# Kernel optimization log

Measured on AMD Instinct MI355X. Metric: run time of the kernel, lower is better.

## Reference

```python
import jax, jax.numpy as jnp
import numpy as np

DIM = 512
NUM_HEADS = 8
HEAD_DIM = DIM // NUM_HEADS
LN_EPS = 1e-5


def setup_inputs() -> dict:
    key = jax.random.key(0)
    k1, k2, k3 = jax.random.split(key, 3)
    x = jax.random.normal(k1, (8, DIM, 32, 32), dtype=jnp.float32)
    # torch Linear default init scale ~ 1/sqrt(fan_in); keep values sane
    w_qkv = jax.random.normal(k2, (3 * DIM, DIM), dtype=jnp.float32) * (DIM ** -0.5)
    b_qkv = jax.random.normal(k3, (3 * DIM,), dtype=jnp.float32) * 0.01
    ln_gamma = jnp.ones((DIM,), dtype=jnp.float32)
    ln_beta = jnp.zeros((DIM,), dtype=jnp.float32)
    return {"x": x, "w_qkv": w_qkv, "b_qkv": b_qkv, "ln_gamma": ln_gamma, "ln_beta": ln_beta}


def _rotate_half(t):
    t1, t2 = jnp.split(t, 2, axis=-1)
    return jnp.concatenate((-t2, t1), axis=-1)


def reference(x, w_qkv, b_qkv, ln_gamma, ln_beta):
    B, C, H, W = x.shape
    N = H * W
    nh, hd = NUM_HEADS, HEAD_DIM
    scale = hd ** -0.5

    # [B, N, C]
    xt = x.reshape(B, C, N).transpose(0, 2, 1)

    # LayerNorm over channel dim
    mu = jnp.mean(xt, axis=-1, keepdims=True)
    var = jnp.mean(jnp.square(xt - mu), axis=-1, keepdims=True)
    xn = (xt - mu) * jax.lax.rsqrt(var + LN_EPS) * ln_gamma + ln_beta

    # QKV projection: [B, N, 3C]
    qkv = xn @ w_qkv.T + b_qkv
    qkv = qkv.reshape(B, N, 3, nh, hd).transpose(2, 0, 3, 1, 4)  # [3, B, nh, N, hd]
    q, k, v = qkv[0], qkv[1], qkv[2]

    # RoPE tables
    freqs = 1.0 / (10000.0 ** (jnp.arange(0, hd, 2, dtype=jnp.float32) / hd))
    pos = jnp.arange(N, dtype=jnp.float32)
    sinusoid = jnp.einsum('i,j->ij', pos, freqs)  # [N, hd/2]
    sin = jnp.repeat(jnp.sin(sinusoid), 2, axis=-1)[None, None]  # [1,1,N,hd]
    cos = jnp.repeat(jnp.cos(sinusoid), 2, axis=-1)[None, None]

    q = q * cos + _rotate_half(q) * sin
    k = k * cos + _rotate_half(k) * sin

    # Full softmax attention: [B, nh, N, N]
    attn = jnp.einsum('bhqd,bhkd->bhqk', q, k) * scale
    attn = jax.nn.softmax(attn, axis=-1)
    out = jnp.einsum('bhqk,bhkd->bhqd', attn, v)  # [B, nh, N, hd]

    out = out.transpose(0, 2, 1, 3).reshape(B, N, C)  # [B, N, C]
    # dropout=0 (eval): identity
    return out.transpose(0, 2, 1).reshape(B, C, H, W)
```

## Files before the change

kernel.cpp:

```cpp
#include <hip/hip_runtime.h>
#include <hip/hip_bf16.h>
#include <math.h>

using bf16 = __hip_bfloat16;
typedef __attribute__((ext_vector_type(8))) short short8;
typedef __attribute__((ext_vector_type(4))) short short4_;
typedef __attribute__((ext_vector_type(4))) float floatx4;

#define C_DIM   512
#define N_TOK   1024
#define NHEAD   8
#define HDIM    64
#define LN_EPSF 1e-5f

__device__ __forceinline__ unsigned short f2b(float f) {
    union { float f; unsigned int u; } v; v.f = f;
    unsigned int r = v.u + 0x7FFFu + ((v.u >> 16) & 1u);
    return (unsigned short)(r >> 16);
}
__device__ __forceinline__ float b2f(unsigned short u) {
    union { unsigned int i; float f; } v; v.i = ((unsigned int)u) << 16; return v.f;
}

__global__ __launch_bounds__(256) void prep_kernel(
        const float* __restrict__ x, const float* __restrict__ w,
        float* __restrict__ mu, float* __restrict__ rsig,
        float* __restrict__ sc, unsigned short* __restrict__ wf) {
    __shared__ float red_s[4][64];
    __shared__ float red_q[4][64];
    const int bx = blockIdx.x;
    const int t  = threadIdx.x;
    if (bx < 128) {
        const int rl = t & 63;
        const int cg = t >> 6;
        const int r0 = bx * 64;
        const int b  = r0 >> 10;
        const int n  = (r0 & 1023) + rl;
        const float* xp = x + (size_t)b * C_DIM * N_TOK + n;
        float s = 0.f, q = 0.f;
        #pragma unroll 4
        for (int i = 0; i < 128; ++i) {
            float v = xp[(size_t)(cg * 128 + i) * N_TOK];
            s += v; q += v * v;
        }
        red_s[cg][rl] = s; red_q[cg][rl] = q;
        __syncthreads();
        if (cg == 0) {
            float S = red_s[0][rl] + red_s[1][rl] + red_s[2][rl] + red_s[3][rl];
            float Q = red_q[0][rl] + red_q[1][rl] + red_q[2][rl] + red_q[3][rl];
            float m   = S * (1.0f / C_DIM);
            float var = Q * (1.0f / C_DIM) - m * m;
            mu[r0 + rl]   = m;
            rsig[r0 + rl] = rsqrtf(var + LN_EPSF);
        }
    } else if (bx < 256) {
        const int idx = (bx - 128) * 256 + t;
        const int n = idx >> 5, f = idx & 31;
        const float fr = __expf((float)f * (-9.210340371976184f / 32.0f));
        float sv, cv;
        sincosf((float)n * fr, &sv, &cv);
        ((float2*)sc)[idx] = make_float2(sv, cv);
    } else {
        const int id   = (bx - 256) * 256 + t;
        const int lane = id & 63;
        const int ksl  = (id >> 6) & 15;
        const int j16  = id >> 10;
        const int c    = lane & 15;
        const int quad = lane >> 4;
        const float* wp = w + (size_t)(j16 * 16 + c) * C_DIM + ksl * 32 + quad * 8;
        const float4 w0 = *(const float4*)(wp);
        const float4 w1 = *(const float4*)(wp + 4);
        short8 pk;
        pk[0] = (short)f2b(w0.x); pk[1] = (short)f2b(w0.y);
        pk[2] = (short)f2b(w0.z); pk[3] = (short)f2b(w0.w);
        pk[4] = (short)f2b(w1.x); pk[5] = (short)f2b(w1.y);
        pk[6] = (short)f2b(w1.z); pk[7] = (short)f2b(w1.w);
        *(short8*)(wf + (size_t)id * 8) = pk;
    }
}

__global__ __launch_bounds__(256) void xnt_kernel(
        const float* __restrict__ x, const float* __restrict__ gamma,
        const float* __restrict__ beta, const float* __restrict__ mu,
        const float* __restrict__ rsig, unsigned short* __restrict__ xnf) {
    __shared__ short Sx[64][72];
    const int t  = threadIdx.x;
    const int c0 = blockIdx.x * 64;
    const int n0 = blockIdx.y * 64;
    const int b  = blockIdx.z;

    const int nq  = t & 15;
    const int crl = t >> 4;
    const int tok = b * N_TOK + n0 + nq * 4;
    const float4 m4 = *(const float4*)(mu + tok);
    const float4 r4 = *(const float4*)(rsig + tok);
    #pragma unroll
    for (int p = 0; p < 4; ++p) {
        const int c = c0 + p * 16 + crl;
        const float g = gamma[c], bt = beta[c];
        const float4 xv = *(const float4*)(x + (size_t)b * C_DIM * N_TOK + (size_t)c * N_TOK + n0 + nq * 4);
        Sx[nq * 4 + 0][p * 16 + crl] = (short)f2b((xv.x - m4.x) * r4.x * g + bt);
        Sx[nq * 4 + 1][p * 16 + crl] = (short)f2b((xv.y - m4.y) * r4.y * g + bt);
        Sx[nq * 4 + 2][p * 16 + crl] = (short)f2b((xv.z - m4.z) * r4.z * g + bt);
        Sx[nq * 4 + 3][p * 16 + crl] = (short)f2b((xv.w - m4.w) * r4.w * g + bt);
    }
    __syncthreads();
    const int wv   = t >> 6;
    const int lane = t & 63;
    const int cfr  = lane & 15;
    const int quad = lane >> 4;
    const int g16  = b * 64 + ((n0 >> 4) + wv);
    #pragma unroll
    for (int ks = 0; ks < 2; ++ks) {
        short8 v = *(const short8*)&Sx[wv * 16 + cfr][ks * 32 + quad * 8];
        *(short8*)(xnf + (((size_t)g16 * 16 + (c0 >> 5) + ks) * 64 + lane) * 8) = v;
    }
}

__global__ __launch_bounds__(256) void qkv_mfma_kernel(
        const unsigned short* __restrict__ xnf, const unsigned short* __restrict__ wf,
        const float* __restrict__ bias, const float* __restrict__ sc,
        unsigned short* __restrict__ qfr, unsigned short* __restrict__ kfr,
        unsigned short* __restrict__ vfr) {
    __shared__ short Es[4][64][72];

    const int t    = threadIdx.x;
    const int wv   = t >> 6;
    const int lane = t & 63;
    const int cl   = lane & 15;
    const int quad = lane >> 4;
    const int t0   = blockIdx.x * 128 + (wv & 1) * 64;
    const int j0w  = blockIdx.y * 128 + (wv >> 1) * 64;
    const int which = j0w >> 9;
    const int h     = (j0w >> 6) & 7;
    const int b     = t0 >> 10;
    const int n0q   = t0 & 1023;
    const int bh    = b * NHEAD + h;

    const unsigned short* ap = xnf + (size_t)(t0 >> 4) * 8192 + lane * 8;
    const unsigned short* bp = wf  + (size_t)(j0w >> 4) * 8192 + lane * 8;

    floatx4 acc[4][4];
    #pragma unroll
    for (int i = 0; i < 4; ++i)
        #pragma unroll
        for (int j = 0; j < 4; ++j) acc[i][j] = (floatx4){0.f, 0.f, 0.f, 0.f};

    #pragma unroll 2
    for (int kt = 0; kt < 16; ++kt) {
        short8 af[4], bfr[4];
        #pragma unroll
        for (int tt = 0; tt < 4; ++tt) af[tt]  = *(const short8*)(ap + ((size_t)tt * 16 + kt) * 512);
        #pragma unroll
        for (int jt = 0; jt < 4; ++jt) bfr[jt] = *(const short8*)(bp + ((size_t)jt * 16 + kt) * 512);
        #pragma unroll
        for (int tt = 0; tt < 4; ++tt)
            #pragma unroll
            for (int jt = 0; jt < 4; ++jt)
                acc[tt][jt] = __builtin_amdgcn_mfma_f32_16x16x32_bf16(af[tt], bfr[jt], acc[tt][jt], 0, 0, 0);
    }

    float bj[4];
    #pragma unroll
    for (int jt = 0; jt < 4; ++jt) bj[jt] = bias[j0w + jt * 16 + cl];
    #pragma unroll
    for (int tt = 0; tt < 4; ++tt)
        #pragma unroll
        for (int jt = 0; jt < 4; ++jt)
            #pragma unroll
            for (int r = 0; r < 4; ++r)
                Es[wv][tt * 16 + quad * 4 + r][jt * 16 + cl] = (short)f2b(acc[tt][jt][r] + bj[jt]);

    if (which == 2) {
        unsigned short* vfb = vfr + ((size_t)bh * 16 + (n0q >> 6)) * 4096;
        #pragma unroll
        for (int dt = 0; dt < 4; ++dt) {
            #pragma unroll
            for (int ks = 0; ks < 2; ++ks) {
                short8 pk;
                #pragma unroll
                for (int j = 0; j < 8; ++j)
                    pk[j] = Es[wv][ks * 32 + quad * 8 + j][dt * 16 + cl];
                *(short8*)(vfb + (((size_t)dt * 2 + ks) * 64 + lane) * 8) = pk;
            }
        }
    } else {
        const float oscale = (which == 0) ? 0.125f : 1.0f;
        unsigned short* base = (which == 0)
            ? qfr + ((size_t)bh * 64 + (n0q >> 4)) * 1024
            : kfr + ((size_t)bh * 16 + (n0q >> 6)) * 4096;
        #pragma unroll
        for (int mt = 0; mt < 4; ++mt) {
            const int n = n0q + mt * 16 + cl;
            const float* scp = sc + ((size_t)n * 32 + quad * 4) * 2;
            #pragma unroll
            for (int ks = 0; ks < 2; ++ks) {
                const short8 v8 = *(const short8*)&Es[wv][mt * 16 + cl][ks * 32 + quad * 8];
                const short8 p8 = *(const short8*)&Es[wv][mt * 16 + cl][(ks ^ 1) * 32 + quad * 8];
                const float* sp = scp + ks * 32;
                const float4 s0 = *(const float4*)sp;
                const float4 s1 = *(const float4*)(sp + 4);
                const float sv[4] = {s0.x, s0.z, s1.x, s1.z};
                const float cv[4] = {s0.y, s0.w, s1.y, s1.w};
                const float sgn = ks ? 1.0f : -1.0f;
                short8 pk;
                #pragma unroll
                for (int j = 0; j < 8; ++j) {
                    const int f = j >> 1;
                    const float val = b2f((unsigned short)v8[j]);
                    const float par = b2f((unsigned short)p8[j]);
                    pk[j] = (short)f2b((val * cv[f] + sgn * par * sv[f]) * oscale);
                }
                *(short8*)(base + (((size_t)mt * 2 + ks) * 64 + lane) * 8) = pk;
            }
        }
    }
}

__global__ __launch_bounds__(256, 2) void attn_mfma_kernel(
        const unsigned short* __restrict__ qfr, const unsigned short* __restrict__ kfr,
        const unsigned short* __restrict__ vfr, float* __restrict__ out) {
    __shared__ __align__(16) short Plds[4][2][16][72];

    const int t    = threadIdx.x;
    const int wv   = t >> 6;
    const int lane = t & 63;
    const int c    = lane & 15;
    const int quad = lane >> 4;
    const int i    = blockIdx.x;
    const int bh   = (i & 7) * 8 + ((i >> 3) & 7);
    const int q32  = (i >> 6) * 4 + wv;
    const int b    = bh >> 3, h = bh & 7;

    const unsigned short* qp   = qfr + ((size_t)bh * 64 + q32 * 2) * 1024 + lane * 8;
    const unsigned short* kraw = kfr + (size_t)bh * 65536 + lane * 8;
    const unsigned short* vraw = vfr + (size_t)bh * 65536 + lane * 8;

    short8 qf[2][2];
    qf[0][0] = *(const short8*)(qp);
    qf[0][1] = *(const short8*)(qp + 512);
    qf[1][0] = *(const short8*)(qp + 1024);
    qf[1][1] = *(const short8*)(qp + 1536);

    floatx4 o_acc[4][2];
    float l_acc[2] = {0.f, 0.f};
    #pragma unroll
    for (int dt = 0; dt < 4; ++dt) {
        o_acc[dt][0] = (floatx4){0.f, 0.f, 0.f, 0.f};
        o_acc[dt][1] = (floatx4){0.f, 0.f, 0.f, 0.f};
    }

    short8 kfA[4][2], vfA[4][2], kfB[4][2], vfB[4][2];

    auto loadf = [&](short8 (&kf)[4][2], short8 (&vf)[4][2], int kt) {
        const unsigned short* kc = kraw + (size_t)kt * 4096;
        const unsigned short* vc = vraw + (size_t)kt * 4096;
        #pragma unroll
        for (int mt = 0; mt < 4; ++mt)
            #pragma unroll
            for (int ks = 0; ks < 2; ++ks) {
                kf[mt][ks] = *(const short8*)(kc + (mt * 2 + ks) * 512);
                vf[mt][ks] = *(const short8*)(vc + (mt * 2 + ks) * 512);
            }
    };

    auto step = [&](short8 (&kf)[4][2], short8 (&vf)[4][2]) {
        floatx4 st[4][2];
        #pragma unroll
        for (int mt = 0; mt < 4; ++mt)
            #pragma unroll
            for (int u = 0; u < 2; ++u) {
                floatx4 z = (floatx4){0.f, 0.f, 0.f, 0.f};
                z = __builtin_amdgcn_mfma_f32_16x16x32_bf16(kf[mt][0], qf[u][0], z, 0, 0, 0);
                st[mt][u] = __builtin_amdgcn_mfma_f32_16x16x32_bf16(kf[mt][1], qf[u][1], z, 0, 0, 0);
            }

        #pragma unroll
        for (int u = 0; u < 2; ++u)
            #pragma unroll
            for (int mt = 0; mt < 4; ++mt) {
                const float e0 = __expf(st[mt][u][0] - 16.0f);
                const float e1 = __expf(st[mt][u][1] - 16.0f);
                const float e2 = __expf(st[mt][u][2] - 16.0f);
                const float e3 = __expf(st[mt][u][3] - 16.0f);
                l_acc[u] += (e0 + e1) + (e2 + e3);
                short4_ pk;
                pk.x = (short)f2b(e0); pk.y = (short)f2b(e1);
                pk.z = (short)f2b(e2); pk.w = (short)f2b(e3);
                *(short4_*)&Plds[wv][u][c][mt * 16 + quad * 4] = pk;
            }

        #pragma unroll
        for (int u = 0; u < 2; ++u) {
            const short8 pf0 = *(const short8*)&Plds[wv][u][c][quad * 8];
            const short8 pf1 = *(const short8*)&Plds[wv][u][c][32 + quad * 8];
            #pragma unroll
            for (int dt = 0; dt < 4; ++dt) {
                o_acc[dt][u] = __builtin_amdgcn_mfma_f32_16x16x32_bf16(vf[dt][0], pf0, o_acc[dt][u], 0, 0, 0);
                o_acc[dt][u] = __builtin_amdgcn_mfma_f32_16x16x32_bf16(vf[dt][1], pf1, o_acc[dt][u], 0, 0, 0);
            }
        }
    };

    loadf(kfA, vfA, 0);
    #pragma unroll 1
    for (int kt = 0; kt < 16; kt += 2) {
        loadf(kfB, vfB, kt + 1);
        step(kfA, vfA);
        if (kt + 2 < 16) loadf(kfA, vfA, kt + 2);
        step(kfB, vfB);
    }

    #pragma unroll
    for (int u = 0; u < 2; ++u) {
        float l = l_acc[u];
        l += __shfl_xor(l, 16);
        l += __shfl_xor(l, 32);
        const float inv = 1.0f / l;
        const int qcol = (q32 * 2 + u) * 16 + c;
        #pragma unroll
        for (int dt = 0; dt < 4; ++dt)
            #pragma unroll
            for (int r = 0; r < 4; ++r) {
                const int d = dt * 16 + quad * 4 + r;
                out[((size_t)b * C_DIM + h * HDIM + d) * N_TOK + qcol] = o_acc[dt][u][r] * inv;
            }
    }
}

extern "C" void kernel_launch(void* const* d_in, const int* in_sizes, int n_in,
                              void* d_out, int out_size, void* d_ws, size_t ws_size,
                              hipStream_t stream) {
    const float* x     = (const float*)d_in[0];
    const float* w     = (const float*)d_in[1];
    const float* bias  = (const float*)d_in[2];
    const float* gamma = (const float*)d_in[3];
    const float* beta  = (const float*)d_in[4];
    float* out = (float*)d_out;

    char* ws = (char*)d_ws;
    float* mu   = (float*)ws;
    float* rsig = (float*)(ws + 32768);
    unsigned short* qfr = (unsigned short*)(ws + 65536);
    unsigned short* kfr = (unsigned short*)(ws + 65536 + 8388608);
    unsigned short* vfr = (unsigned short*)(ws + 65536 + 16777216);
    unsigned short* xnf = (unsigned short*)(ws + 65536 + 25165824);
    unsigned short* wf  = (unsigned short*)(ws + 65536 + 33554432);
    float* sc           = (float*)(ws + 65536 + 35127296);

    hipLaunchKernelGGL(prep_kernel, dim3(640), dim3(256), 0, stream, x, w, mu, rsig, sc, wf);
    hipLaunchKernelGGL(xnt_kernel, dim3(8, 16, 8), dim3(256), 0, stream,
                       x, gamma, beta, mu, rsig, xnf);
    hipLaunchKernelGGL(qkv_mfma_kernel, dim3(64, 12), dim3(256), 0, stream,
                       xnf, wf, bias, sc, qfr, kfr, vfr);
    hipLaunchKernelGGL(attn_mfma_kernel, dim3(512), dim3(256), 0, stream, qfr, kfr, vfr, out);
}
```

Baseline: 141.9 us.

## Use hardware bf16 pack, exp2 softmax, folded q-scale and MFMA priority hints

Replaces the manual round-to-nearest bf16 conversions with the v_cvt_pk_bf16_f32 instruction across the prep, projection and attention kernels. The softmax exponent now uses the native exp2 builtin on a fused multiply-add of the log2(e) scaling and the constant shift. The query scale is folded into the bias epilogue, and the RoPE step uses fmaf. Raises wave priority around the MFMA blocks with s_setprio so matrix issue gets precedence over the exp and pack work of other waves. These changes aim to cut VALU instruction count in the attention inner loop and the epilogues. They may slightly change rounding, and the q scale is now applied before bf16 rounding and RoPE rather than after.

Measured after the change: 139.0 us. -2.1%, faster.

```diff
diff --git a/kernel.cpp b/kernel.cpp
--- a/kernel.cpp
+++ b/kernel.cpp
@@ -4,8 +4,9 @@
 
 using bf16 = __hip_bfloat16;
 typedef __attribute__((ext_vector_type(8))) short short8;
-typedef __attribute__((ext_vector_type(4))) short short4_;
 typedef __attribute__((ext_vector_type(4))) float floatx4;
+typedef __attribute__((ext_vector_type(4))) unsigned int uint4_;
+typedef __attribute__((ext_vector_type(2))) unsigned int uint2_;
 
 #define C_DIM   512
 #define N_TOK   1024
@@ -20,6 +21,14 @@
 }
 __device__ __forceinline__ float b2f(unsigned short u) {
     union { unsigned int i; float f; } v; v.i = ((unsigned int)u) << 16; return v.f;
+}
+__device__ __forceinline__ unsigned int cvt_pk_bf16(float lo, float hi) {
+    unsigned int r;
+    asm("v_cvt_pk_bf16_f32 %0, %1, %2" : "=v"(r) : "v"(lo), "v"(hi));
+    return r;
+}
+__device__ __forceinline__ float fast_exp2(float x) {
+    return __builtin_amdgcn_exp2f(x);
 }
 
 __global__ __launch_bounds__(256) void prep_kernel(
@@ -70,12 +79,12 @@
         const float* wp = w + (size_t)(j16 * 16 + c) * C_DIM + ksl * 32 + quad * 8;
         const float4 w0 = *(const float4*)(wp);
         const float4 w1 = *(const float4*)(wp + 4);
-        short8 pk;
-        pk[0] = (short)f2b(w0.x); pk[1] = (short)f2b(w0.y);
-        pk[2] = (short)f2b(w0.z); pk[3] = (short)f2b(w0.w);
-        pk[4] = (short)f2b(w1.x); pk[5] = (short)f2b(w1.y);
-        pk[6] = (short)f2b(w1.z); pk[7] = (short)f2b(w1.w);
-        *(short8*)(wf + (size_t)id * 8) = pk;
+        uint4_ pk;
+        pk.x = cvt_pk_bf16(w0.x, w0.y);
+        pk.y = cvt_pk_bf16(w0.z, w0.w);
+        pk.z = cvt_pk_bf16(w1.x, w1.y);
+        pk.w = cvt_pk_bf16(w1.z, w1.w);
+        *(uint4_*)(wf + (size_t)id * 8) = pk;
     }
 }
 
@@ -160,16 +169,17 @@
                 acc[tt][jt] = __builtin_amdgcn_mfma_f32_16x16x32_bf16(af[tt], bfr[jt], acc[tt][jt], 0, 0, 0);
     }
 
+    const float os = (which == 0) ? 0.125f : 1.0f;
     float bj[4];
     #pragma unroll
-    for (int jt = 0; jt < 4; ++jt) bj[jt] = bias[j0w + jt * 16 + cl];
+    for (int jt = 0; jt < 4; ++jt) bj[jt] = bias[j0w + jt * 16 + cl] * os;
     #pragma unroll
     for (int tt = 0; tt < 4; ++tt)
         #pragma unroll
         for (int jt = 0; jt < 4; ++jt)
             #pragma unroll
             for (int r = 0; r < 4; ++r)
-                Es[wv][tt * 16 + quad * 4 + r][jt * 16 + cl] = (short)f2b(acc[tt][jt][r] + bj[jt]);
+                Es[wv][tt * 16 + quad * 4 + r][jt * 16 + cl] = (short)f2b(fmaf(acc[tt][jt][r], os, bj[jt]));
 
     if (which == 2) {
         unsigned short* vfb = vfr + ((size_t)bh * 16 + (n0q >> 6)) * 4096;
@@ -185,7 +195,6 @@
             }
         }
     } else {
-        const float oscale = (which == 0) ? 0.125f : 1.0f;
         unsigned short* base = (which == 0)
             ? qfr + ((size_t)bh * 64 + (n0q >> 4)) * 1024
             : kfr + ((size_t)bh * 16 + (n0q >> 6)) * 4096;
@@ -203,15 +212,20 @@
                 const float sv[4] = {s0.x, s0.z, s1.x, s1.z};
                 const float cv[4] = {s0.y, s0.w, s1.y, s1.w};
                 const float sgn = ks ? 1.0f : -1.0f;
-                short8 pk;
+                uint4_ pk;
+                unsigned int pw[4];
                 #pragma unroll
-                for (int j = 0; j < 8; ++j) {
-                    const int f = j >> 1;
-                    const float val = b2f((unsigned short)v8[j]);
-                    const float par = b2f((unsigned short)p8[j]);
-                    pk[j] = (short)f2b((val * cv[f] + sgn * par * sv[f]) * oscale);
+                for (int f = 0; f < 4; ++f) {
+                    const float svs = sgn * sv[f];
+                    const float a0 = b2f((unsigned short)v8[2 * f]);
+                    const float a1 = b2f((unsigned short)v8[2 * f + 1]);
+                    const float p0 = b2f((unsigned short)p8[2 * f]);
+                    const float p1 = b2f((unsigned short)p8[2 * f + 1]);
+                    pw[f] = cvt_pk_bf16(fmaf(p0, svs, a0 * cv[f]),
+                                        fmaf(p1, svs, a1 * cv[f]));
                 }
-                *(short8*)(base + (((size_t)mt * 2 + ks) * 64 + lane) * 8) = pk;
+                pk.x = pw[0]; pk.y = pw[1]; pk.z = pw[2]; pk.w = pw[3];
+                *(uint4_*)(base + (((size_t)mt * 2 + ks) * 64 + lane) * 8) = pk;
             }
         }
     }
@@ -250,6 +264,9 @@
         o_acc[dt][1] = (floatx4){0.f, 0.f, 0.f, 0.f};
     }
 
+    const float LOG2E  = 1.4426950408889634f;
+    const float ESHIFT = -23.083120654223414f;
+
     short8 kfA[4][2], vfA[4][2], kfB[4][2], vfB[4][2];
 
     auto loadf = [&](short8 (&kf)[4][2], short8 (&vf)[4][2], int kt) {
@@ -266,6 +283,7 @@
 
     auto step = [&](short8 (&kf)[4][2], short8 (&vf)[4][2]) {
         floatx4 st[4][2];
+        __builtin_amdgcn_s_setprio(1);
         #pragma unroll
         for (int mt = 0; mt < 4; ++mt)
             #pragma unroll
@@ -274,31 +292,34 @@
                 z = __builtin_amdgcn_mfma_f32_16x16x32_bf16(kf[mt][0], qf[u][0], z, 0, 0, 0);
                 st[mt][u] = __builtin_amdgcn_mfma_f32_16x16x32_bf16(kf[mt][1], qf[u][1], z, 0, 0, 0);
             }
+        __builtin_amdgcn_s_setprio(0);
 
         #pragma unroll
         for (int u = 0; u < 2; ++u)
             #pragma unroll
             for (int mt = 0; mt < 4; ++mt) {
-                const float e0 = __expf(st[mt][u][0] - 16.0f);
-                const float e1 = __expf(st[mt][u][1] - 16.0f);
-                const float e2 = __expf(st[mt][u][2] - 16.0f);
-                const float e3 = __expf(st[mt][u][3] - 16.0f);
+                const float e0 = fast_exp2(fmaf(st[mt][u][0], LOG2E, ESHIFT));
+                const float e1 = fast_exp2(fmaf(st[mt][u][1], LOG2E, ESHIFT));
+                const float e2 = fast_exp2(fmaf(st[mt][u][2], LOG2E, ESHIFT));
+                const float e3 = fast_exp2(fmaf(st[mt][u][3], LOG2E, ESHIFT));
                 l_acc[u] += (e0 + e1) + (e2 + e3);
-                short4_ pk;
-                pk.x = (short)f2b(e0); pk.y = (short)f2b(e1);
-                pk.z = (short)f2b(e2); pk.w = (short)f2b(e3);
-                *(short4_*)&Plds[wv][u][c][mt * 16 + quad * 4] = pk;
+                uint2_ pk;
+                pk.x = cvt_pk_bf16(e0, e1);
+                pk.y = cvt_pk_bf16(e2, e3);
+                *(uint2_*)&Plds[wv][u][c][mt * 16 + quad * 4] = pk;
             }
 
         #pragma unroll
         for (int u = 0; u < 2; ++u) {
             const short8 pf0 = *(const short8*)&Plds[wv][u][c][quad * 8];
             const short8 pf1 = *(const short8*)&Plds[wv][u][c][32 + quad * 8];
+            __builtin_amdgcn_s_setprio(1);
             #pragma unroll
             for (int dt = 0; dt < 4; ++dt) {
                 o_acc[dt][u] = __builtin_amdgcn_mfma_f32_16x16x32_bf16(vf[dt][0], pf0, o_acc[dt][u], 0, 0, 0);
                 o_acc[dt][u] = __builtin_amdgcn_mfma_f32_16x16x32_bf16(vf[dt][1], pf1, o_acc[dt][u], 0, 0, 0);
             }
+            __builtin_amdgcn_s_setprio(0);
         }
     };
 
```
